# Optimization experiments

Measured on AMD Instinct MI355X. Metric: run time of the kernel, lower is better.

The kernel has to match this reference:

```python
import jax, jax.numpy as jnp
import numpy as np

N_CELLS = 100000
N_ISO = 16
K_PLUS_1 = 31  # self + 30 neighbors, per sklearn kneighbors convention


def setup_inputs() -> dict:
    key = jax.random.key(0)
    k1, k2, k3, k4, k5 = jax.random.split(key, 5)
    return {
        "unsplice": jax.random.normal(k1, (N_CELLS,), dtype=jnp.float32),
        "splices": jax.random.normal(k2, (N_CELLS, N_ISO), dtype=jnp.float32),
        "unsplice_predict": jax.random.normal(k3, (N_CELLS,), dtype=jnp.float32),
        "splice_predicts": jax.random.normal(k4, (N_CELLS, N_ISO), dtype=jnp.float32),
        "indices": jax.random.randint(k5, (N_CELLS, K_PLUS_1), 0, N_CELLS, dtype=jnp.int64),
    }


def reference(unsplice, splices, unsplice_predict, splice_predicts, indices):
    # Velocity vector per cell in (1 + n_isoforms)-dim space: v = (du, ds_1..ds_K)
    uv = unsplice_predict - unsplice                      # [N]
    sv = splice_predicts - splices                        # [N, I]
    v = jnp.concatenate([uv[:, None], sv], axis=1)        # [N, D], D = I+1

    nbr = indices[:, 1:]                                  # [N, K] drop self
    # Neighbor displacement vectors vn[i,k] = x[nbr[i,k]] - x[i]
    un = unsplice[nbr] - unsplice[:, None]                # [N, K]
    sn = splices[nbr] - splices[:, None, :]               # [N, K, I]
    vn = jnp.concatenate([un[..., None], sn], axis=-1)    # [N, K, D]

    dots = jnp.einsum('nd,nkd->nk', v, vn)                # [N, K]
    vi_norm = jnp.linalg.norm(v, axis=1)                  # [N]
    vn_norm = jnp.linalg.norm(vn, axis=2)                 # [N, K]
    denom = vi_norm[:, None] * vn_norm
    denom = jnp.where(denom == 0, jnp.ones_like(denom), denom)
    cos_sim = dots / denom                                # [N, K]
    cost = 1.0 - jnp.max(cos_sim, axis=1)                 # [N]
    return jnp.mean(cost)
```

## Files before the change

### kernel.cpp

```cpp
#include <hip/hip_runtime.h>
#include <math.h>

#define N_CELLS_C 100000
#define N_ISO_C 16
#define KP1_C 31
#define BLOCK 256

typedef _Float16 hf2 __attribute__((ext_vector_type(2)));
union Rec16 { float4 f; hf2 h[4]; };

__device__ __forceinline__ float fdot2f(hf2 a, hf2 b, float c) {
    return __builtin_amdgcn_fdot2(a, b, c, false);
}

__device__ __forceinline__ int idx_shift(const char* idx_bytes) {
    const int lane = threadIdx.x & 63;
    int probe = 0;
    if (lane < 16) probe = ((const int*)idx_bytes)[2 * lane + 1];
    return __any(probe != 0) ? 2 : 3;
}

__global__ __launch_bounds__(BLOCK) void pack_kernel(
    const float* __restrict__ unsplice,
    const float* __restrict__ splices,
    char* __restrict__ rec,
    _Float16* __restrict__ u16)
{
    const int t = blockIdx.x * BLOCK + threadIdx.x;
    const int cell = t >> 1, h = t & 1;
    if (cell >= N_CELLS_C) return;
    const float* srow = splices + (long long)cell * N_ISO_C + 8 * h;
    const float4 a = *(const float4*)srow;
    const float4 b = *(const float4*)(srow + 4);
    Rec16 r;
    r.h[0] = hf2{(_Float16)a.x, (_Float16)a.y};
    r.h[1] = hf2{(_Float16)a.z, (_Float16)a.w};
    r.h[2] = hf2{(_Float16)b.x, (_Float16)b.y};
    r.h[3] = hf2{(_Float16)b.z, (_Float16)b.w};
    *(float4*)(rec + ((long long)cell << 5) + (h << 4)) = r.f;
    if (h == 0) u16[cell] = (_Float16)unsplice[cell];
}

__global__ __launch_bounds__(BLOCK) void cost_kernel_h(
    const float* __restrict__ unsplice,
    const float* __restrict__ splices,
    const float* __restrict__ unsplice_predict,
    const float* __restrict__ splice_predicts,
    const char*  __restrict__ idx_bytes,
    const char*  __restrict__ rec,
    const _Float16* __restrict__ u16,
    float*       __restrict__ partials)
{
    const int tid  = threadIdx.x;
    const int sub  = tid & 7;
    const int w    = sub & 1;
    const int h    = sub >> 1;
    const int cell = blockIdx.x * (BLOCK / 8) + (tid >> 3);
    const int shift = idx_shift(idx_bytes);

    const float* srow = splices         + (long long)cell * N_ISO_C + 8 * w;
    const float* prow = splice_predicts + (long long)cell * N_ISO_C + 8 * w;
    const float4 a  = *(const float4*)srow,  b  = *(const float4*)(srow + 4);
    const float4 pa = *(const float4*)prow,  pb = *(const float4*)(prow + 4);
    const hf2 c0{(_Float16)a.x,  (_Float16)a.y},  c1{(_Float16)a.z,  (_Float16)a.w};
    const hf2 c2{(_Float16)b.x,  (_Float16)b.y},  c3{(_Float16)b.z,  (_Float16)b.w};
    const hf2 q0{(_Float16)pa.x, (_Float16)pa.y}, q1{(_Float16)pa.z, (_Float16)pa.w};
    const hf2 q2{(_Float16)pb.x, (_Float16)pb.y}, q3{(_Float16)pb.z, (_Float16)pb.w};
    const hf2 v0 = q0 - c0, v1 = q1 - c1, v2 = q2 - c2, v3 = q3 - c3;

    const float u_i = (float)(_Float16)unsplice[cell];
    const float uv  = unsplice_predict[cell] - unsplice[cell];

    float vp = fdot2f(v0, v0, fdot2f(v1, v1, fdot2f(v2, v2, fdot2f(v3, v3, 0.f))));
    vp += __shfl_xor(vp, 1);
    const float vn2 = vp + uv * uv;
    const float inv_vi = (vn2 > 0.f) ? rsqrtf(vn2) : 0.f;

    const long long base = (long long)cell * KP1_C;
    int jv[8];
    #pragma unroll
    for (int t = 0; t < 8; ++t) {
        int k = 1 + h + 4 * t;
        if (k > 30) k = 30;
        jv[t] = *(const int*)(idx_bytes + ((base + k) << shift));
    }

    float maxq = -INFINITY;
    #pragma unroll
    for (int t = 0; t < 8; ++t) {
        const int j = jv[t];
        const float u_j = (float)u16[j];
        const Rec16 g = *(const Rec16*)(rec + ((long long)j << 5) + (w << 4));
        const hf2 d0 = g.h[0] - c0;
        const hf2 d1 = g.h[1] - c1;
        const hf2 d2 = g.h[2] - c2;
        const hf2 d3 = g.h[3] - c3;
        float dp = fdot2f(v0, d0, fdot2f(v1, d1, fdot2f(v2, d2, fdot2f(v3, d3, 0.f))));
        float np = fdot2f(d0, d0, fdot2f(d1, d1, fdot2f(d2, d2, fdot2f(d3, d3, 0.f))));
        dp += __shfl_xor(dp, 1);
        np += __shfl_xor(np, 1);
        const float un  = u_j - u_i;
        const float dot = dp + uv * un;
        const float nn2 = np + un * un;
        const float rn  = (nn2 > 0.f) ? rsqrtf(nn2) : 0.f;
        maxq = fmaxf(maxq, dot * rn);
    }
    maxq = fmaxf(maxq, __shfl_xor(maxq, 2));
    maxq = fmaxf(maxq, __shfl_xor(maxq, 4));

    float cost = (sub == 0) ? (1.0f - maxq * inv_vi) : 0.f;

    for (int off = 32; off > 0; off >>= 1) cost += __shfl_down(cost, off);
    __shared__ float wsum[BLOCK / 64];
    if ((tid & 63) == 0) wsum[tid >> 6] = cost;
    __syncthreads();
    if (tid == 0) {
        float s = 0.f;
        #pragma unroll
        for (int wv = 0; wv < BLOCK / 64; ++wv) s += wsum[wv];
        partials[blockIdx.x] = s;
    }
}

__global__ __launch_bounds__(BLOCK) void cost_kernel_f32(
    const float* __restrict__ unsplice,
    const float* __restrict__ splices,
    const float* __restrict__ unsplice_predict,
    const float* __restrict__ splice_predicts,
    const char*  __restrict__ idx_bytes,
    float*       __restrict__ partials)
{
    const int tid  = threadIdx.x;
    const int q    = tid & 3;
    const int cell = blockIdx.x * (BLOCK / 4) + (tid >> 2);
    const int shift = idx_shift(idx_bytes);

    float cost = 0.0f;
    if (cell < N_CELLS_C) {
        const float u_i = unsplice[cell];
        const float uv  = unsplice_predict[cell] - u_i;
        const float4 s4  = *(const float4*)(splices         + (long long)cell * N_ISO_C + 4 * q);
        const float4 sp4 = *(const float4*)(splice_predicts + (long long)cell * N_ISO_C + 4 * q);
        const float v0 = sp4.x - s4.x, v1 = sp4.y - s4.y, v2 = sp4.z - s4.z, v3 = sp4.w - s4.w;
        float vpp = v0*v0 + v1*v1 + v2*v2 + v3*v3;
        vpp += __shfl_xor(vpp, 1);
        vpp += __shfl_xor(vpp, 2);
        const float vn2 = vpp + uv * uv;
        const float inv_vi = (vn2 > 0.0f) ? rsqrtf(vn2) : 0.0f;
        const long long base = (long long)cell * KP1_C;
        float maxq = -INFINITY;
        #pragma unroll
        for (int k = 1; k < KP1_C; ++k) {
            const int j = *(const int*)(idx_bytes + ((base + k) << shift));
            const float unj = unsplice[j];
            const float4 n4 = *(const float4*)(splices + (long long)j * N_ISO_C + 4 * q);
            const float d0 = n4.x - s4.x, d1 = n4.y - s4.y, d2 = n4.z - s4.z, d3 = n4.w - s4.w;
            float dp = v0*d0 + v1*d1 + v2*d2 + v3*d3;
            float np = d0*d0 + d1*d1 + d2*d2 + d3*d3;
            dp += __shfl_xor(dp, 1);  np += __shfl_xor(np, 1);
            dp += __shfl_xor(dp, 2);  np += __shfl_xor(np, 2);
            const float un  = unj - u_i;
            const float dot = dp + uv * un;
            const float nn2 = np + un * un;
            const float rn  = (nn2 > 0.0f) ? rsqrtf(nn2) : 0.0f;
            maxq = fmaxf(maxq, dot * rn);
        }
        if (q == 0) cost = 1.0f - maxq * inv_vi;
    }
    for (int off = 32; off > 0; off >>= 1) cost += __shfl_down(cost, off);
    __shared__ float wsum[BLOCK / 64];
    if ((tid & 63) == 0) wsum[tid >> 6] = cost;
    __syncthreads();
    if (tid == 0) {
        float s = 0.0f;
        #pragma unroll
        for (int wv = 0; wv < BLOCK / 64; ++wv) s += wsum[wv];
        partials[blockIdx.x] = s;
    }
}

__global__ __launch_bounds__(BLOCK) void final_reduce_kernel(
    const float* __restrict__ partials, int nparts, float* __restrict__ out)
{
    float s = 0.0f;
    for (int i = threadIdx.x; i < nparts; i += BLOCK) s += partials[i];
    for (int off = 32; off > 0; off >>= 1) s += __shfl_down(s, off);
    __shared__ float wsum[BLOCK / 64];
    if ((threadIdx.x & 63) == 0) wsum[threadIdx.x >> 6] = s;
    __syncthreads();
    if (threadIdx.x == 0) {
        float t = 0.0f;
        #pragma unroll
        for (int wv = 0; wv < BLOCK / 64; ++wv) t += wsum[wv];
        out[0] = t / (float)N_CELLS_C;
    }
}

extern "C" void kernel_launch(void* const* d_in, const int* in_sizes, int n_in,
                              void* d_out, int out_size, void* d_ws, size_t ws_size,
                              hipStream_t stream) {
    const float* unsplice         = (const float*)d_in[0];
    const float* splices          = (const float*)d_in[1];
    const float* unsplice_predict = (const float*)d_in[2];
    const float* splice_predicts  = (const float*)d_in[3];
    const char*  idx_bytes        = (const char*)d_in[4];
    float* out = (float*)d_out;

    char*      rec      = (char*)d_ws;
    _Float16*  u16      = (_Float16*)((char*)d_ws + (size_t)N_CELLS_C * 32);
    float*     partials = (float*)((char*)d_ws + 3400000);

    const size_t req = 3400000 + 4 * 4096;

    if (ws_size >= req) {
        const int pack_blocks = (2 * N_CELLS_C + BLOCK - 1) / BLOCK;
        pack_kernel<<<pack_blocks, BLOCK, 0, stream>>>(unsplice, splices, rec, u16);
        const int nblocks = N_CELLS_C / (BLOCK / 8);
        cost_kernel_h<<<nblocks, BLOCK, 0, stream>>>(
            unsplice, splices, unsplice_predict, splice_predicts,
            idx_bytes, rec, u16, partials);
        final_reduce_kernel<<<1, BLOCK, 0, stream>>>(partials, nblocks, out);
    } else {
        float* fb_partials = (float*)d_ws;
        const int nblocks = (N_CELLS_C + (BLOCK / 4) - 1) / (BLOCK / 4);
        cost_kernel_f32<<<nblocks, BLOCK, 0, stream>>>(
            unsplice, splices, unsplice_predict, splice_predicts,
            idx_bytes, fb_partials);
        final_reduce_kernel<<<1, BLOCK, 0, stream>>>(fb_partials, nblocks, out);
    }
}
```

Baseline: 47.37 us.

## Pack neighbor records into 32-byte 14-bit floats with fused unsplice

Neighbor data (16 splices plus unsplice) is now packed into a single 32-byte record per cell using a truncated 14-bit half-precision code, replacing the separate 32-byte fp16 record and 2-byte fp16 unsplice array. The cost kernel switches from 8 threads per cell to 4 threads per cell, each handling 8 neighbors in full fp32 with two batched gathers. The aim is fewer random gather transactions, since each neighbor now needs one aligned 32-byte read instead of two scattered reads. In exchange it adds bit-unpacking ALU work and lower precision, with 12 mantissa-equivalent bits dropped to 8.

```diff
diff --git a/kernel.cpp b/kernel.cpp
--- a/kernel.cpp
+++ b/kernel.cpp
@@ -5,13 +5,7 @@
 #define N_ISO_C 16
 #define KP1_C 31
 #define BLOCK 256
-
-typedef _Float16 hf2 __attribute__((ext_vector_type(2)));
-union Rec16 { float4 f; hf2 h[4]; };
-
-__device__ __forceinline__ float fdot2f(hf2 a, hf2 b, float c) {
-    return __builtin_amdgcn_fdot2(a, b, c, false);
-}
+#define CPB 64
 
 __device__ __forceinline__ int idx_shift(const char* idx_bytes) {
     const int lane = threadIdx.x & 63;
@@ -20,95 +14,119 @@
     return __any(probe != 0) ? 2 : 3;
 }
 
+__device__ __forceinline__ unsigned enc14(float x) {
+    const _Float16 h = (_Float16)x;
+    const unsigned short b = __builtin_bit_cast(unsigned short, h);
+    return (((unsigned)b + 2u) >> 2) & 0x3FFFu;
+}
+__device__ __forceinline__ float dec14(unsigned v) {
+    const unsigned short b = (unsigned short)(v << 2);
+    const _Float16 h = __builtin_bit_cast(_Float16, b);
+    return (float)h;
+}
+
 __global__ __launch_bounds__(BLOCK) void pack_kernel(
     const float* __restrict__ unsplice,
     const float* __restrict__ splices,
-    char* __restrict__ rec,
-    _Float16* __restrict__ u16)
-{
-    const int t = blockIdx.x * BLOCK + threadIdx.x;
-    const int cell = t >> 1, h = t & 1;
+    unsigned* __restrict__ rec)
+{
+    const int cell = blockIdx.x * BLOCK + threadIdx.x;
     if (cell >= N_CELLS_C) return;
-    const float* srow = splices + (long long)cell * N_ISO_C + 8 * h;
-    const float4 a = *(const float4*)srow;
-    const float4 b = *(const float4*)(srow + 4);
-    Rec16 r;
-    r.h[0] = hf2{(_Float16)a.x, (_Float16)a.y};
-    r.h[1] = hf2{(_Float16)a.z, (_Float16)a.w};
-    r.h[2] = hf2{(_Float16)b.x, (_Float16)b.y};
-    r.h[3] = hf2{(_Float16)b.z, (_Float16)b.w};
-    *(float4*)(rec + ((long long)cell << 5) + (h << 4)) = r.f;
-    if (h == 0) u16[cell] = (_Float16)unsplice[cell];
-}
-
-__global__ __launch_bounds__(BLOCK) void cost_kernel_h(
+    const float4* row = (const float4*)(splices + (long long)cell * N_ISO_C);
+    const float4 r0 = row[0], r1 = row[1], r2 = row[2], r3 = row[3];
+    float vals[17] = { r0.x, r0.y, r0.z, r0.w, r1.x, r1.y, r1.z, r1.w,
+                       r2.x, r2.y, r2.z, r2.w, r3.x, r3.y, r3.z, r3.w,
+                       unsplice[cell] };
+    unsigned w[8] = {0, 0, 0, 0, 0, 0, 0, 0};
+    #pragma unroll
+    for (int i = 0; i < 17; ++i) {
+        const unsigned v = enc14(vals[i]);
+        const int s = 14 * i, k = s >> 5, off = s & 31;
+        w[k] |= v << off;
+        if (off > 18) w[k + 1] |= v >> (32 - off);
+    }
+    uint4* dst = (uint4*)(rec + (size_t)cell * 8);
+    dst[0] = uint4{w[0], w[1], w[2], w[3]};
+    dst[1] = uint4{w[4], w[5], w[6], w[7]};
+}
+
+__global__ __launch_bounds__(BLOCK) void cost_kernel(
     const float* __restrict__ unsplice,
     const float* __restrict__ splices,
     const float* __restrict__ unsplice_predict,
     const float* __restrict__ splice_predicts,
     const char*  __restrict__ idx_bytes,
-    const char*  __restrict__ rec,
-    const _Float16* __restrict__ u16,
+    const unsigned* __restrict__ rec,
     float*       __restrict__ partials)
 {
     const int tid  = threadIdx.x;
-    const int sub  = tid & 7;
-    const int w    = sub & 1;
-    const int h    = sub >> 1;
-    const int cell = blockIdx.x * (BLOCK / 8) + (tid >> 3);
+    const int q    = tid & 3;
+    const int cell = blockIdx.x * CPB + (tid >> 2);
     const int shift = idx_shift(idx_bytes);
 
-    const float* srow = splices         + (long long)cell * N_ISO_C + 8 * w;
-    const float* prow = splice_predicts + (long long)cell * N_ISO_C + 8 * w;
-    const float4 a  = *(const float4*)srow,  b  = *(const float4*)(srow + 4);
-    const float4 pa = *(const float4*)prow,  pb = *(const float4*)(prow + 4);
-    const hf2 c0{(_Float16)a.x,  (_Float16)a.y},  c1{(_Float16)a.z,  (_Float16)a.w};
-    const hf2 c2{(_Float16)b.x,  (_Float16)b.y},  c3{(_Float16)b.z,  (_Float16)b.w};
-    const hf2 q0{(_Float16)pa.x, (_Float16)pa.y}, q1{(_Float16)pa.z, (_Float16)pa.w};
-    const hf2 q2{(_Float16)pb.x, (_Float16)pb.y}, q3{(_Float16)pb.z, (_Float16)pb.w};
-    const hf2 v0 = q0 - c0, v1 = q1 - c1, v2 = q2 - c2, v3 = q3 - c3;
-
-    const float u_i = (float)(_Float16)unsplice[cell];
-    const float uv  = unsplice_predict[cell] - unsplice[cell];
-
-    float vp = fdot2f(v0, v0, fdot2f(v1, v1, fdot2f(v2, v2, fdot2f(v3, v3, 0.f))));
-    vp += __shfl_xor(vp, 1);
-    const float vn2 = vp + uv * uv;
-    const float inv_vi = (vn2 > 0.f) ? rsqrtf(vn2) : 0.f;
-
-    const long long base = (long long)cell * KP1_C;
-    int jv[8];
-    #pragma unroll
-    for (int t = 0; t < 8; ++t) {
-        int k = 1 + h + 4 * t;
-        if (k > 30) k = 30;
-        jv[t] = *(const int*)(idx_bytes + ((base + k) << shift));
-    }
-
-    float maxq = -INFINITY;
-    #pragma unroll
-    for (int t = 0; t < 8; ++t) {
-        const int j = jv[t];
-        const float u_j = (float)u16[j];
-        const Rec16 g = *(const Rec16*)(rec + ((long long)j << 5) + (w << 4));
-        const hf2 d0 = g.h[0] - c0;
-        const hf2 d1 = g.h[1] - c1;
-        const hf2 d2 = g.h[2] - c2;
-        const hf2 d3 = g.h[3] - c3;
-        float dp = fdot2f(v0, d0, fdot2f(v1, d1, fdot2f(v2, d2, fdot2f(v3, d3, 0.f))));
-        float np = fdot2f(d0, d0, fdot2f(d1, d1, fdot2f(d2, d2, fdot2f(d3, d3, 0.f))));
-        dp += __shfl_xor(dp, 1);
-        np += __shfl_xor(np, 1);
-        const float un  = u_j - u_i;
-        const float dot = dp + uv * un;
-        const float nn2 = np + un * un;
-        const float rn  = (nn2 > 0.f) ? rsqrtf(nn2) : 0.f;
-        maxq = fmaxf(maxq, dot * rn);
-    }
-    maxq = fmaxf(maxq, __shfl_xor(maxq, 2));
-    maxq = fmaxf(maxq, __shfl_xor(maxq, 4));
-
-    float cost = (sub == 0) ? (1.0f - maxq * inv_vi) : 0.f;
+    float cost = 0.0f;
+    if (cell < N_CELLS_C) {
+        float ci[17], v[17];
+        {
+            const float4* sr = (const float4*)(splices         + (long long)cell * N_ISO_C);
+            const float4* pr = (const float4*)(splice_predicts + (long long)cell * N_ISO_C);
+            #pragma unroll
+            for (int b = 0; b < 4; ++b) {
+                const float4 s4 = sr[b], p4 = pr[b];
+                ci[4*b+0] = s4.x; ci[4*b+1] = s4.y; ci[4*b+2] = s4.z; ci[4*b+3] = s4.w;
+                v[4*b+0] = p4.x - s4.x; v[4*b+1] = p4.y - s4.y;
+                v[4*b+2] = p4.z - s4.z; v[4*b+3] = p4.w - s4.w;
+            }
+            ci[16] = unsplice[cell];
+            v[16]  = unsplice_predict[cell] - ci[16];
+        }
+        float vn2 = 0.f;
+        #pragma unroll
+        for (int i = 0; i < 17; ++i) vn2 = fmaf(v[i], v[i], vn2);
+        const float inv_vi = (vn2 > 0.f) ? rsqrtf(vn2) : 0.f;
+
+        const long long base = (long long)cell * KP1_C;
+        int jv[8];
+        #pragma unroll
+        for (int t = 0; t < 8; ++t) {
+            int k = 1 + q + 4 * t;
+            if (k > 30) k = 30;
+            jv[t] = *(const int*)(idx_bytes + ((base + k) << shift));
+        }
+
+        float maxq = -INFINITY;
+        #pragma unroll
+        for (int c2 = 0; c2 < 2; ++c2) {
+            uint4 ga[4], gb[4];
+            #pragma unroll
+            for (int t = 0; t < 4; ++t) {
+                const uint4* p = (const uint4*)(rec + (size_t)jv[c2 * 4 + t] * 8);
+                ga[t] = p[0];
+                gb[t] = p[1];
+            }
+            #pragma unroll
+            for (int t = 0; t < 4; ++t) {
+                const unsigned w[8] = { ga[t].x, ga[t].y, ga[t].z, ga[t].w,
+                                        gb[t].x, gb[t].y, gb[t].z, gb[t].w };
+                float dot = 0.f, nn2 = 0.f;
+                #pragma unroll
+                for (int i = 0; i < 17; ++i) {
+                    const int s = 14 * i, k = s >> 5, off = s & 31;
+                    unsigned raw = w[k] >> off;
+                    if (off > 18) raw |= w[k + 1] << (32 - off);
+                    const float g = dec14(raw & 0x3FFFu);
+                    const float d = g - ci[i];
+                    dot = fmaf(v[i], d, dot);
+                    nn2 = fmaf(d, d, nn2);
+                }
+                const float rn = (nn2 > 0.f) ? rsqrtf(nn2) : 0.f;
+                maxq = fmaxf(maxq, dot * rn);
+            }
+        }
+        maxq = fmaxf(maxq, __shfl_xor(maxq, 1));
+        maxq = fmaxf(maxq, __shfl_xor(maxq, 2));
+        if (q == 0) cost = 1.0f - maxq * inv_vi;
+    }
 
     for (int off = 32; off > 0; off >>= 1) cost += __shfl_down(cost, off);
     __shared__ float wsum[BLOCK / 64];
@@ -206,19 +224,18 @@
     const char*  idx_bytes        = (const char*)d_in[4];
     float* out = (float*)d_out;
 
-    char*      rec      = (char*)d_ws;
-    _Float16*  u16      = (_Float16*)((char*)d_ws + (size_t)N_CELLS_C * 32);
-    float*     partials = (float*)((char*)d_ws + 3400000);
-
-    const size_t req = 3400000 + 4 * 4096;
+    unsigned* rec      = (unsigned*)d_ws;
+    float*    partials = (float*)((char*)d_ws + 3200000);
+
+    const size_t req = 3200000 + 8 * 4096;
 
     if (ws_size >= req) {
-        const int pack_blocks = (2 * N_CELLS_C + BLOCK - 1) / BLOCK;
-        pack_kernel<<<pack_blocks, BLOCK, 0, stream>>>(unsplice, splices, rec, u16);
-        const int nblocks = N_CELLS_C / (BLOCK / 8);
-        cost_kernel_h<<<nblocks, BLOCK, 0, stream>>>(
+        const int pack_blocks = (N_CELLS_C + BLOCK - 1) / BLOCK;
+        pack_kernel<<<pack_blocks, BLOCK, 0, stream>>>(unsplice, splices, rec);
+        const int nblocks = (N_CELLS_C + CPB - 1) / CPB;
+        cost_kernel<<<nblocks, BLOCK, 0, stream>>>(
             unsplice, splices, unsplice_predict, splice_predicts,
-            idx_bytes, rec, u16, partials);
+            idx_bytes, rec, partials);
         final_reduce_kernel<<<1, BLOCK, 0, stream>>>(partials, nblocks, out);
     } else {
         float* fb_partials = (float*)d_ws;
```

Result: faster. 41.15 us (-13.1%).
